# Optimization experiments

Measured on AMD Instinct MI355X. Metric: run time of the kernel, lower is better.

## Reference

```python
import jax, jax.numpy as jnp
import numpy as np
import math

D = 1024        # d_model
H = 16          # n_head
HD = D // H     # head_dim = 64
NKV = H // 4    # n_kv_heads = 4
SPARSE_K = 64
TEMP = 1.0      # sparse_gate_temp (selection softmax temp; importance unused for output)
EPS = 1e-8


def rmsnorm(x, w):
    return x * jax.lax.rsqrt(jnp.mean(x * x, axis=-1, keepdims=True) + EPS) * w


def alibi_bias(n_head, T):
    # slopes = 2 ** (-(arange(H)/(H-1) * 8)); bias = -slope * |i - j|
    slopes = 2.0 ** (-(jnp.arange(n_head, dtype=jnp.float32) / (n_head - 1) * 8.0))
    pos = jnp.arange(T)
    dist = jnp.abs(pos[:, None] - pos[None, :]).astype(jnp.float32)
    return -slopes[:, None, None] * dist[None, :, :]  # (H, T, T)


def setup_inputs() -> dict:
    key = jax.random.key(0)
    ks = jax.random.split(key, 8)
    B, T = 1, 2048
    s = 0.02
    return {
        "x": jax.random.normal(ks[0], (B, T, D), dtype=jnp.float32),
        "wq": jax.random.normal(ks[1], (D, H * HD), dtype=jnp.float32) * s,
        "bq": jnp.zeros((H * HD,), dtype=jnp.float32),
        "wkv": jax.random.normal(ks[2], (D, 2 * NKV * HD), dtype=jnp.float32) * s,
        "bkv": jnp.zeros((2 * NKV * HD,), dtype=jnp.float32),
        "wo": jax.random.normal(ks[3], (H * HD, D), dtype=jnp.float32) * s,
        "bo": jnp.zeros((D,), dtype=jnp.float32),
        "qn_w": jnp.ones((HD,), dtype=jnp.float32),
        "kn_w": jnp.ones((HD,), dtype=jnp.float32),
    }


def reference(x, wq, bq, wkv, bkv, wo, bo, qn_w, kn_w):
    B, T, C = x.shape
    scale = 1.0 / math.sqrt(HD)

    # projections -> (B, H, T, HD)
    q = (x @ wq + bq).reshape(B, T, H, HD).transpose(0, 2, 1, 3)
    kv = (x @ wkv + bkv).reshape(B, T, 2, NKV, HD)
    k = kv[:, :, 0].transpose(0, 2, 1, 3)  # (B, NKV, T, HD)
    v = kv[:, :, 1].transpose(0, 2, 1, 3)

    q = rmsnorm(q, qn_w)
    k = rmsnorm(k, kn_w)

    # GQA: repeat kv heads to full head count
    rep = H // NKV
    k = jnp.repeat(k, rep, axis=1)  # (B, H, T, HD)
    v = jnp.repeat(v, rep, axis=1)

    bias = alibi_bias(H, T)                             # (H, T, T)
    causal = jnp.triu(jnp.ones((T, T), dtype=bool), 1)  # True above diagonal

    # ---- selection pass (no-grad in original) ----
    pre = jnp.einsum('bhqd,bhkd->bhqk', q, k) * scale + bias[None]
    pre = jnp.where(causal, -jnp.inf, pre)
    kk = min(SPARSE_K, T)
    _, topk_idx = jax.lax.top_k(pre, kk)                # (B, H, T, kk)

    # scatter top-k indices into a boolean sparse mask
    bi = jnp.arange(B)[:, None, None, None]
    hi = jnp.arange(H)[None, :, None, None]
    ti = jnp.arange(T)[None, None, :, None]
    sparse_mask = jnp.zeros((B, H, T, T), dtype=bool).at[bi, hi, ti, topk_idx].set(True)

    # ---- real attention pass ----
    att = jnp.einsum('bhqd,bhkd->bhqk', q, k) * scale + bias[None]
    att = jnp.where(causal[None, None] | ~sparse_mask, -jnp.inf, att)
    att = jax.nn.softmax(att, axis=-1)

    y = jnp.einsum('bhqk,bhkd->bhqd', att, v)
    y = y.transpose(0, 2, 1, 3).reshape(B, T, C)
    return y @ wo + bo
```

## Files before the change

### kernel.cpp

```cpp
#include <hip/hip_runtime.h>
#include <hip/hip_bf16.h>
#include <stdint.h>

#define TSEQ   2048
#define DMODEL 1024
#define NH     16
#define HDIM   64
#define NKVH   4

typedef __attribute__((ext_vector_type(8))) short short8;
typedef __attribute__((ext_vector_type(8))) _Float16 half8;
typedef __attribute__((ext_vector_type(4))) float f32x4;
typedef __hip_bfloat16 bf16;

__device__ __forceinline__ void gload16(const void* g, void* l) {
    __builtin_amdgcn_global_load_lds(
        (const __attribute__((address_space(1))) uint32_t*)g,
        (__attribute__((address_space(3))) uint32_t*)l, 16, 0, 0);
}

__device__ __forceinline__ uint32_t packkey(float s, int idx) {
    uint32_t fb = __float_as_uint(s);
    uint32_t mono = fb ^ (uint32_t)(((int)fb >> 31) | 0x80000000);
    return (mono & 0xFFFFF800u) | (uint32_t)(2047 - idx);
}
__device__ __forceinline__ float unpacks(uint32_t key) {
    uint32_t mono = key & 0xFFFFF800u;
    uint32_t fb = (mono & 0x80000000u) ? (mono ^ 0x80000000u) : ~mono;
    return __uint_as_float(fb);
}
__device__ __forceinline__ int unpacki(uint32_t key) {
    return 2047 - (int)(key & 0x7FFu);
}

__device__ __forceinline__ void bsortK(uint32_t& kk, int lane) {
#pragma unroll
    for (int k = 2; k <= 64; k <<= 1) {
#pragma unroll
        for (int j = k >> 1; j > 0; j >>= 1) {
            uint32_t o = (uint32_t)__shfl_xor((int)kk, j, 64);
            bool wmin = ((lane & j) == 0) == ((lane & k) == 0);
            kk = wmin ? min(kk, o) : max(kk, o);
        }
    }
}
__device__ __forceinline__ void bmergeK(uint32_t& kk, int lane) {
#pragma unroll
    for (int j = 32; j > 0; j >>= 1) {
        uint32_t o = (uint32_t)__shfl_xor((int)kk, j, 64);
        kk = ((lane & j) == 0) ? min(kk, o) : max(kk, o);
    }
}

__global__ __launch_bounds__(256) void prep_kernel(
    const float* __restrict__ x, const float* __restrict__ wq,
    const float* __restrict__ wkv, const float* __restrict__ wo,
    bf16* __restrict__ cx, bf16* __restrict__ cwqT,
    bf16* __restrict__ cwkvT, bf16* __restrict__ cwoT)
{
    __shared__ float tile[32][33];
    const int bid = blockIdx.x;
    if (bid < 1024) {
        const size_t i0 = (size_t)bid * 256 + threadIdx.x;
        for (size_t i = i0; i < 2097152; i += 262144) cx[i] = __float2bfloat16(x[i]);
        return;
    }
    const float* in; bf16* out; int R, Cc, bx, by;
    if (bid < 2048) {
        int idx = bid - 1024; in = wq; out = cwqT; R = 1024; Cc = 1024;
        bx = (idx & 31) << 5; by = (idx >> 5) << 5;
    } else if (bid < 2560) {
        int idx = bid - 2048; in = wkv; out = cwkvT; R = 1024; Cc = 512;
        bx = (idx & 15) << 5; by = (idx >> 4) << 5;
    } else {
        int idx = bid - 2560; in = wo; out = cwoT; R = 1024; Cc = 1024;
        bx = (idx & 31) << 5; by = (idx >> 5) << 5;
    }
    const int tx = threadIdx.x & 31, ty = threadIdx.x >> 5;
#pragma unroll
    for (int i = 0; i < 32; i += 8)
        tile[ty + i][tx] = in[(size_t)(by + ty + i) * Cc + bx + tx];
    __syncthreads();
#pragma unroll
    for (int i = 0; i < 32; i += 8)
        out[(size_t)(bx + ty + i) * R + by + tx] = __float2bfloat16(tile[tx][ty + i]);
}

__global__ __launch_bounds__(256) void gemm_qkv(
    const bf16* __restrict__ A, const bf16* __restrict__ BTq,
    const bf16* __restrict__ BTkv, const float* __restrict__ bq,
    const float* __restrict__ bkv, _Float16* __restrict__ qh,
    _Float16* __restrict__ kh, float* __restrict__ vbuf,
    const float* __restrict__ qn_w, const float* __restrict__ kn_w)
{
    __shared__ short As[64][64];
    __shared__ short Bs[64][64];
    const int tid = threadIdx.x;
    const int bx = blockIdx.x;
    const bool isQ = bx < 16;
    const bf16* BT = isQ ? BTq : BTkv;
    const float* bias = isQ ? bq : bkv;
    const float* wn = isQ ? qn_w : kn_w;
    const int n0 = (isQ ? bx : bx - 16) * 64;
    const int K = 1024;
    const int m0 = blockIdx.y * 64;
    const int w = tid >> 6, lane = tid & 63;
    const int q4 = lane >> 4, mm = lane & 15;
    f32x4 acc[4];
#pragma unroll
    for (int nb = 0; nb < 4; ++nb) acc[nb] = (f32x4){0.f, 0.f, 0.f, 0.f};

    const int ar = tid >> 3;
    const int sslot = (tid & 7) ^ (ar & 7);
    const short* Ag = (const short*)A + (size_t)(m0 + ar) * K + sslot * 8;
    const short* Ag2 = (const short*)A + (size_t)(m0 + ar + 32) * K + ((tid & 7) ^ ((ar + 32) & 7)) * 8;
    const short* Bg = (const short*)BT + (size_t)(n0 + ar) * K + sslot * 8;
    const short* Bg2 = (const short*)BT + (size_t)(n0 + ar + 32) * K + ((tid & 7) ^ ((ar + 32) & 7)) * 8;

    const int xm = mm & 7;
    const short* Asf = (const short*)As;
    const short* Bsf = (const short*)Bs;
    const int aoff0 = (w * 16 + mm) * 64 + ((q4 ^ xm)) * 8;
    const int aoff1 = (w * 16 + mm) * 64 + (((4 + q4) ^ xm)) * 8;
    int boff0[4], boff1[4];
#pragma unroll
    for (int nb = 0; nb < 4; ++nb) {
        boff0[nb] = (nb * 16 + mm) * 64 + ((q4 ^ xm)) * 8;
        boff1[nb] = (nb * 16 + mm) * 64 + (((4 + q4) ^ xm)) * 8;
    }

    for (int k0 = 0; k0 < K; k0 += 64) {
        __syncthreads();
        gload16(Ag + k0, &As[ar][(tid & 7) * 8]);
        gload16(Ag2 + k0, &As[ar + 32][(tid & 7) * 8]);
        gload16(Bg + k0, &Bs[ar][(tid & 7) * 8]);
        gload16(Bg2 + k0, &Bs[ar + 32][(tid & 7) * 8]);
        __syncthreads();
        short8 af0 = *(const short8*)(Asf + aoff0);
        short8 af1 = *(const short8*)(Asf + aoff1);
#pragma unroll
        for (int nb = 0; nb < 4; ++nb) {
            short8 b0 = *(const short8*)(Bsf + boff0[nb]);
            short8 b1 = *(const short8*)(Bsf + boff1[nb]);
            acc[nb] = __builtin_amdgcn_mfma_f32_16x16x32_bf16(af0, b0, acc[nb], 0, 0, 0);
            acc[nb] = __builtin_amdgcn_mfma_f32_16x16x32_bf16(af1, b1, acc[nb], 0, 0, 0);
        }
    }

    float vv[4][4];
#pragma unroll
    for (int nb = 0; nb < 4; ++nb)
#pragma unroll
        for (int r = 0; r < 4; ++r)
            vv[nb][r] = acc[nb][r] + bias[n0 + nb * 16 + mm];

    if (isQ || n0 < 256) {
#pragma unroll
        for (int r = 0; r < 4; ++r) {
            float ss = 0.f;
#pragma unroll
            for (int nb = 0; nb < 4; ++nb) ss += vv[nb][r] * vv[nb][r];
#pragma unroll
            for (int j = 8; j >= 1; j >>= 1) ss += __shfl_xor(ss, j, 64);
            float rs = 1.0f / sqrtf(ss * (1.0f / 64.0f) + 1e-8f);
            int row = m0 + w * 16 + q4 * 4 + r;
            if (isQ) {
#pragma unroll
                for (int nb = 0; nb < 4; ++nb) {
                    int d = nb * 16 + mm;
                    qh[(size_t)row * DMODEL + n0 + d] =
                        (_Float16)(vv[nb][r] * rs * wn[d] * 0.125f);
                }
            } else {
                int kvh = n0 >> 6;
#pragma unroll
                for (int nb = 0; nb < 4; ++nb) {
                    int d = nb * 16 + mm;
                    kh[((size_t)kvh * TSEQ + row) * HDIM + d] =
                        (_Float16)(vv[nb][r] * rs * wn[d]);
                }
            }
        }
    } else {
        int kvh = (n0 - 256) >> 6;
#pragma unroll
        for (int r = 0; r < 4; ++r) {
            int row = m0 + w * 16 + q4 * 4 + r;
#pragma unroll
            for (int nb = 0; nb < 4; ++nb)
                vbuf[((size_t)kvh * TSEQ + row) * HDIM + nb * 16 + mm] = vv[nb][r];
        }
    }
}

__global__ __launch_bounds__(256) void gemm_out(
    const bf16* __restrict__ A, const bf16* __restrict__ BT,
    const float* __restrict__ bias, float* __restrict__ C, int M, int N, int K)
{
    __shared__ short As[64][64];
    __shared__ short Bs[64][64];
    const int tid = threadIdx.x;
    const int m0 = blockIdx.y * 64, n0 = blockIdx.x * 64;
    const int w = tid >> 6, lane = tid & 63;
    const int q4 = lane >> 4, mm = lane & 15;
    f32x4 acc[4];
#pragma unroll
    for (int nb = 0; nb < 4; ++nb) acc[nb] = (f32x4){0.f, 0.f, 0.f, 0.f};

    const int ar = tid >> 3;
    const int sslot = (tid & 7) ^ (ar & 7);
    const short* Ag = (const short*)A + (size_t)(m0 + ar) * K + sslot * 8;
    const short* Ag2 = (const short*)A + (size_t)(m0 + ar + 32) * K + ((tid & 7) ^ ((ar + 32) & 7)) * 8;
    const short* Bg = (const short*)BT + (size_t)(n0 + ar) * K + sslot * 8;
    const short* Bg2 = (const short*)BT + (size_t)(n0 + ar + 32) * K + ((tid & 7) ^ ((ar + 32) & 7)) * 8;

    const int xm = mm & 7;
    const short* Asf = (const short*)As;
    const short* Bsf = (const short*)Bs;
    const int aoff0 = (w * 16 + mm) * 64 + ((q4 ^ xm)) * 8;
    const int aoff1 = (w * 16 + mm) * 64 + (((4 + q4) ^ xm)) * 8;
    int boff0[4], boff1[4];
#pragma unroll
    for (int nb = 0; nb < 4; ++nb) {
        boff0[nb] = (nb * 16 + mm) * 64 + ((q4 ^ xm)) * 8;
        boff1[nb] = (nb * 16 + mm) * 64 + (((4 + q4) ^ xm)) * 8;
    }

    for (int k0 = 0; k0 < K; k0 += 64) {
        __syncthreads();
        gload16(Ag + k0, &As[ar][(tid & 7) * 8]);
        gload16(Ag2 + k0, &As[ar + 32][(tid & 7) * 8]);
        gload16(Bg + k0, &Bs[ar][(tid & 7) * 8]);
        gload16(Bg2 + k0, &Bs[ar + 32][(tid & 7) * 8]);
        __syncthreads();
        short8 af0 = *(const short8*)(Asf + aoff0);
        short8 af1 = *(const short8*)(Asf + aoff1);
#pragma unroll
        for (int nb = 0; nb < 4; ++nb) {
            short8 b0 = *(const short8*)(Bsf + boff0[nb]);
            short8 b1 = *(const short8*)(Bsf + boff1[nb]);
            acc[nb] = __builtin_amdgcn_mfma_f32_16x16x32_bf16(af0, b0, acc[nb], 0, 0, 0);
            acc[nb] = __builtin_amdgcn_mfma_f32_16x16x32_bf16(af1, b1, acc[nb], 0, 0, 0);
        }
    }
#pragma unroll
    for (int nb = 0; nb < 4; ++nb)
#pragma unroll
        for (int r = 0; r < 4; ++r)
            C[(size_t)(m0 + w * 16 + q4 * 4 + r) * N + n0 + nb * 16 + mm]
                = acc[nb][r] + bias[n0 + nb * 16 + mm];
}

__global__ __launch_bounds__(256, 8) void attn_kernel(
    const _Float16* __restrict__ qh, const _Float16* __restrict__ kh,
    const float* __restrict__ vbuf, bf16* __restrict__ ybuf,
    const float* __restrict__ kn_w)
{
    __shared__ float    Sg[2][8][68];
    __shared__ uint32_t cbK[8][128];
    __shared__ int      eminS[4];
    const int tid = threadIdx.x;
    const int w = tid >> 6, lane = tid & 63;
    const int mm = lane & 15, q4 = lane >> 4;
    const int h = 15 - (blockIdx.x >> 8);
    const int t0 = (255 - (blockIdx.x & 255)) << 3;
    const int kvh = h >> 2;
    const float slope = exp2f(-((float)h) * (8.0f / 15.0f));
    const _Float16* kbase = kh + (size_t)kvh * TSEQ * HDIM;
    const int nch = (t0 + 7) >> 6;
    const uint32_t PADK   = packkey(-1e30f, 0);
    const uint32_t VALIDT = packkey(-1e29f, 2047);

    float kw = fabsf(kn_w[lane]);
#pragma unroll
    for (int j = 32; j > 0; j >>= 1) kw = fmaxf(kw, __shfl_xor(kw, j, 64));
    const float kfac = 8.0f * kw * 1.001f;

    float Brow[2];
    int em = 0x7fffffff;
#pragma unroll
    for (int rr = 0; rr < 2; ++rr) {
        const int r = 2 * w + rr;
        float qe = (float)qh[(size_t)(t0 + r) * DMODEL + h * HDIM + lane];
        float qs = qe * qe;
#pragma unroll
        for (int j = 32; j > 0; j >>= 1) qs += __shfl_xor(qs, j, 64);
        Brow[rr] = sqrtf(qs) * kfac + 1e-3f;
        float Dw = 2.0f * Brow[rr] / slope + 64.0f;
        int e = (int)floorf((float)(t0 + r) - Dw);
        em = min(em, e);
    }
    if (lane == 0) eminS[w] = em;

    const _Float16* qp = qh + (size_t)(t0 + (mm & 7)) * DMODEL + h * HDIM + q4 * 8;
    half8 qf0 = *(const half8*)(qp);
    half8 qf1 = *(const half8*)(qp + 32);

    {
        const int jb = nch << 6;
        const _Float16* kp = kbase + ((size_t)(jb + w * 16 + mm)) * HDIM + q4 * 8;
        half8 b0 = *(const half8*)(kp);
        half8 b1 = *(const half8*)(kp + 32);
        f32x4 a = __builtin_amdgcn_mfma_f32_16x16x32_f16(
            qf0, b0, (f32x4){0.f, 0.f, 0.f, 0.f}, 0, 0, 0);
        a = __builtin_amdgcn_mfma_f32_16x16x32_f16(qf1, b1, a, 0, 0, 0);
        if (q4 < 2) {
#pragma unroll
            for (int rr = 0; rr < 4; ++rr)
                Sg[0][q4 * 4 + rr][w * 16 + mm] = a[rr];
        }
    }
    __syncthreads();

    int em4 = min(min(eminS[0], eminS[1]), min(eminS[2], eminS[3]));
    const int c_min = (em4 > 0) ? (em4 >> 6) : 0;

    uint32_t csK[2]; uint32_t thK[2]; float thr[2]; int cnt[2];
#pragma unroll
    for (int rr = 0; rr < 2; ++rr) { csK[rr] = PADK; thK[rr] = PADK; thr[rr] = -1e30f; cnt[rr] = 0; }

    int p = 0;
    for (int c = nch; c >= c_min; --c) {
        const int jb = c << 6;
#pragma unroll
        for (int rr = 0; rr < 2; ++rr) {
            const int r = 2 * w + rr;
            int dm = (t0 + r - 63) - jb;
            float dmin = (float)(dm > 0 ? dm : 0);
            if (Brow[rr] - slope * dmin < thr[rr]) continue;
            float sr = Sg[p][r][lane];
            int dist = (t0 + r) - (jb + lane);
            float s = sr - slope * (float)dist;
            uint32_t kc = packkey(s, jb + lane);
            bool pass = (dist >= 0) && (kc >= thK[rr]);
            unsigned long long mk = __ballot(pass);
            if (mk) {
                int rank = __popcll(mk & ((1ull << lane) - 1ull));
                if (pass) cbK[r][cnt[rr] + rank] = kc;
                cnt[rr] += __popcll(mk);
                if (cnt[rr] >= 64) {
                    uint32_t nk = cbK[r][lane];
                    bsortK(nk, lane);
                    uint32_t rv = (uint32_t)__shfl_xor((int)nk, 63, 64);
                    csK[rr] = max(csK[rr], rv);
                    bmergeK(csK[rr], lane);
                    thK[rr] = (uint32_t)__shfl((int)csK[rr], 0, 64);
                    thr[rr] = unpacks(thK[rr]);
                    int rem = cnt[rr] - 64;
                    uint32_t mv = 0u;
                    if (lane < rem) mv = cbK[r][64 + lane];
                    if (lane < rem) cbK[r][lane] = mv;
                    cnt[rr] = rem;
                }
            }
        }
        const int cn = c - 1;
        if (cn >= c_min) {
            const _Float16* kp = kbase + ((size_t)((cn << 6) + w * 16 + mm)) * HDIM + q4 * 8;
            half8 b0 = *(const half8*)(kp);
            half8 b1 = *(const half8*)(kp + 32);
            f32x4 a = __builtin_amdgcn_mfma_f32_16x16x32_f16(
                qf0, b0, (f32x4){0.f, 0.f, 0.f, 0.f}, 0, 0, 0);
            a = __builtin_amdgcn_mfma_f32_16x16x32_f16(qf1, b1, a, 0, 0, 0);
            if (q4 < 2) {
#pragma unroll
                for (int rr = 0; rr < 4; ++rr)
                    Sg[p ^ 1][q4 * 4 + rr][w * 16 + mm] = a[rr];
            }
        }
        p ^= 1;
        __syncthreads();
    }

    const float* vb = vbuf + (size_t)kvh * TSEQ * HDIM + lane;
#pragma unroll
    for (int rr = 0; rr < 2; ++rr) {
        const int r = 2 * w + rr;
        if (cnt[rr] > 0) {
            uint32_t nk = (lane < cnt[rr]) ? cbK[r][lane] : 0u;
            bsortK(nk, lane);
            uint32_t rv = (uint32_t)__shfl_xor((int)nk, 63, 64);
            csK[rr] = max(csK[rr], rv);
            bmergeK(csK[rr], lane);
        }
        uint32_t kk = csK[rr];
        float sx = unpacks((uint32_t)__shfl((int)kk, 63, 64));
        bool valid = kk > VALIDT;
        float s = unpacks(kk);
        float pr = valid ? __expf(s - sx) : 0.f;
        float l = pr;
#pragma unroll
        for (int j2 = 32; j2 > 0; j2 >>= 1) l += __shfl_xor(l, j2, 64);
        float wgt = pr / l;
        int widx = valid ? unpacki(kk) : 0;
        uint32_t g = (__float_as_uint(wgt) & 0xFFFFF800u) | (uint32_t)widx;
        float acc = 0.f;
#pragma unroll 8
        for (int i = 0; i < 64; ++i) {
            uint32_t gb = (uint32_t)__shfl((int)g, i, 64);
            float wv = __uint_as_float(gb & 0xFFFFF800u);
            int  ix = (int)(gb & 0x7FFu);
            acc += wv * vb[(size_t)ix * HDIM];
        }
        ybuf[(size_t)(t0 + r) * DMODEL + h * HDIM + lane] = __float2bfloat16(acc);
    }
}

extern "C" void kernel_launch(void* const* d_in, const int* in_sizes, int n_in,
                              void* d_out, int out_size, void* d_ws, size_t ws_size,
                              hipStream_t stream)
{
    const float* x    = (const float*)d_in[0];
    const float* wq   = (const float*)d_in[1];
    const float* bq   = (const float*)d_in[2];
    const float* wkv  = (const float*)d_in[3];
    const float* bkv  = (const float*)d_in[4];
    const float* wo   = (const float*)d_in[5];
    const float* bo   = (const float*)d_in[6];
    const float* qn_w = (const float*)d_in[7];
    const float* kn_w = (const float*)d_in[8];
    char* ws = (char*)d_ws;
    bf16*      cx    = (bf16*)(ws);
    bf16*      cwqT  = (bf16*)(ws + ((size_t)4  << 20));
    bf16*      cwkvT = (bf16*)(ws + ((size_t)6  << 20));
    bf16*      cwoT  = (bf16*)(ws + ((size_t)7  << 20));
    _Float16*  qh    = (_Float16*)(ws + ((size_t)9  << 20));
    _Float16*  kh    = (_Float16*)(ws + ((size_t)21 << 20));
    float*     vbuf  = (float*)(ws + ((size_t)22 << 20));
    bf16*      ybuf  = (bf16*)(ws + ((size_t)24 << 20));
    float*     out   = (float*)d_out;

    prep_kernel<<<3584, 256, 0, stream>>>(x, wq, wkv, wo, cx, cwqT, cwkvT, cwoT);
    gemm_qkv<<<dim3(24, TSEQ / 64), 256, 0, stream>>>(
        cx, cwqT, cwkvT, bq, bkv, qh, kh, vbuf, qn_w, kn_w);
    attn_kernel<<<NH * (TSEQ / 8), 256, 0, stream>>>(qh, kh, vbuf, ybuf, kn_w);
    gemm_out<<<dim3(DMODEL / 64, TSEQ / 64), 256, 0, stream>>>(
        ybuf, cwoT, bo, out, TSEQ, DMODEL, DMODEL);
}
```

Measured before the change: 187.3 us.

## Make attention selection wave-independent, removing shared score buffer and block barriers

Each wave now computes QK scores for its own two query rows across all four 16-key subtiles with MFMA and redistributes them via shuffles, rather than splitting key subtiles across waves and exchanging scores through double-buffered shared memory. This drops the per-chunk __syncthreads and the shared Sg/eminS arrays. Each wave computes its own lower chunk bound and skips chunks whose bound cannot beat the current top-k threshold. The cost is four times the MFMA and K-load work per wave per chunk, with most MFMA rows unused, plus extra shuffles.

```diff
diff --git a/kernel.cpp b/kernel.cpp
--- a/kernel.cpp
+++ b/kernel.cpp
@@ -256,9 +256,7 @@
     const float* __restrict__ vbuf, bf16* __restrict__ ybuf,
     const float* __restrict__ kn_w)
 {
-    __shared__ float    Sg[2][8][68];
     __shared__ uint32_t cbK[8][128];
-    __shared__ int      eminS[4];
     const int tid = threadIdx.x;
     const int w = tid >> 6, lane = tid & 63;
     const int mm = lane & 15, q4 = lane >> 4;
@@ -270,6 +268,7 @@
     const int nch = (t0 + 7) >> 6;
     const uint32_t PADK   = packkey(-1e30f, 0);
     const uint32_t VALIDT = packkey(-1e29f, 2047);
+    const int rbase = t0 + 2 * w;
 
     float kw = fabsf(kn_w[lane]);
 #pragma unroll
@@ -280,56 +279,55 @@
     int em = 0x7fffffff;
 #pragma unroll
     for (int rr = 0; rr < 2; ++rr) {
-        const int r = 2 * w + rr;
-        float qe = (float)qh[(size_t)(t0 + r) * DMODEL + h * HDIM + lane];
+        float qe = (float)qh[(size_t)(rbase + rr) * DMODEL + h * HDIM + lane];
         float qs = qe * qe;
 #pragma unroll
         for (int j = 32; j > 0; j >>= 1) qs += __shfl_xor(qs, j, 64);
         Brow[rr] = sqrtf(qs) * kfac + 1e-3f;
         float Dw = 2.0f * Brow[rr] / slope + 64.0f;
-        int e = (int)floorf((float)(t0 + r) - Dw);
+        int e = (int)floorf((float)(rbase + rr) - Dw);
         em = min(em, e);
     }
-    if (lane == 0) eminS[w] = em;
-
-    const _Float16* qp = qh + (size_t)(t0 + (mm & 7)) * DMODEL + h * HDIM + q4 * 8;
+    const int c_min = (em > 0) ? (em >> 6) : 0;
+
+    const _Float16* qp = qh + (size_t)(rbase + (mm & 1)) * DMODEL + h * HDIM + q4 * 8;
     half8 qf0 = *(const half8*)(qp);
     half8 qf1 = *(const half8*)(qp + 32);
 
-    {
-        const int jb = nch << 6;
-        const _Float16* kp = kbase + ((size_t)(jb + w * 16 + mm)) * HDIM + q4 * 8;
-        half8 b0 = *(const half8*)(kp);
-        half8 b1 = *(const half8*)(kp + 32);
-        f32x4 a = __builtin_amdgcn_mfma_f32_16x16x32_f16(
-            qf0, b0, (f32x4){0.f, 0.f, 0.f, 0.f}, 0, 0, 0);
-        a = __builtin_amdgcn_mfma_f32_16x16x32_f16(qf1, b1, a, 0, 0, 0);
-        if (q4 < 2) {
-#pragma unroll
-            for (int rr = 0; rr < 4; ++rr)
-                Sg[0][q4 * 4 + rr][w * 16 + mm] = a[rr];
-        }
-    }
-    __syncthreads();
-
-    int em4 = min(min(eminS[0], eminS[1]), min(eminS[2], eminS[3]));
-    const int c_min = (em4 > 0) ? (em4 >> 6) : 0;
-
     uint32_t csK[2]; uint32_t thK[2]; float thr[2]; int cnt[2];
 #pragma unroll
     for (int rr = 0; rr < 2; ++rr) { csK[rr] = PADK; thK[rr] = PADK; thr[rr] = -1e30f; cnt[rr] = 0; }
 
-    int p = 0;
     for (int c = nch; c >= c_min; --c) {
         const int jb = c << 6;
+        int dm0 = (rbase - 63) - jb;
+        float dmin0 = (float)(dm0 > 0 ? dm0 : 0);
+        int dm1 = (rbase + 1 - 63) - jb;
+        float dmin1 = (float)(dm1 > 0 ? dm1 : 0);
+        bool need0 = (Brow[0] - slope * dmin0 >= thr[0]);
+        bool need1 = (Brow[1] - slope * dmin1 >= thr[1]);
+        if (!(need0 || need1)) continue;
+
+        f32x4 a[4];
+#pragma unroll
+        for (int jt = 0; jt < 4; ++jt) {
+            const _Float16* kp = kbase + (size_t)(jb + jt * 16 + mm) * HDIM + q4 * 8;
+            half8 b0 = *(const half8*)(kp);
+            half8 b1 = *(const half8*)(kp + 32);
+            f32x4 t = __builtin_amdgcn_mfma_f32_16x16x32_f16(
+                qf0, b0, (f32x4){0.f, 0.f, 0.f, 0.f}, 0, 0, 0);
+            a[jt] = __builtin_amdgcn_mfma_f32_16x16x32_f16(qf1, b1, t, 0, 0, 0);
+        }
 #pragma unroll
         for (int rr = 0; rr < 2; ++rr) {
             const int r = 2 * w + rr;
-            int dm = (t0 + r - 63) - jb;
-            float dmin = (float)(dm > 0 ? dm : 0);
-            if (Brow[rr] - slope * dmin < thr[rr]) continue;
-            float sr = Sg[p][r][lane];
-            int dist = (t0 + r) - (jb + lane);
+            if (rr == 0 ? !need0 : !need1) continue;
+            float s0 = __shfl(a[0][rr], mm, 64);
+            float s1 = __shfl(a[1][rr], mm, 64);
+            float s2 = __shfl(a[2][rr], mm, 64);
+            float s3 = __shfl(a[3][rr], mm, 64);
+            float sr = (q4 == 0) ? s0 : (q4 == 1) ? s1 : (q4 == 2) ? s2 : s3;
+            int dist = (rbase + rr) - (jb + lane);
             float s = sr - slope * (float)dist;
             uint32_t kc = packkey(s, jb + lane);
             bool pass = (dist >= 0) && (kc >= thK[rr]);
@@ -354,22 +352,6 @@
                 }
             }
         }
-        const int cn = c - 1;
-        if (cn >= c_min) {
-            const _Float16* kp = kbase + ((size_t)((cn << 6) + w * 16 + mm)) * HDIM + q4 * 8;
-            half8 b0 = *(const half8*)(kp);
-            half8 b1 = *(const half8*)(kp + 32);
-            f32x4 a = __builtin_amdgcn_mfma_f32_16x16x32_f16(
-                qf0, b0, (f32x4){0.f, 0.f, 0.f, 0.f}, 0, 0, 0);
-            a = __builtin_amdgcn_mfma_f32_16x16x32_f16(qf1, b1, a, 0, 0, 0);
-            if (q4 < 2) {
-#pragma unroll
-                for (int rr = 0; rr < 4; ++rr)
-                    Sg[p ^ 1][q4 * 4 + rr][w * 16 + mm] = a[rr];
-            }
-        }
-        p ^= 1;
-        __syncthreads();
     }
 
     const float* vb = vbuf + (size_t)kvh * TSEQ * HDIM + lane;
@@ -402,7 +384,7 @@
             int  ix = (int)(gb & 0x7FFu);
             acc += wv * vb[(size_t)ix * HDIM];
         }
-        ybuf[(size_t)(t0 + r) * DMODEL + h * HDIM + lane] = __float2bfloat16(acc);
+        ybuf[(size_t)(rbase + rr) * DMODEL + h * HDIM + lane] = __float2bfloat16(acc);
     }
 }
 
```

Measured after the change: 264.7 us. +41.3%, slower.
